# Kernel tuning notes

Measured on AMD Instinct MI355X. Metric: run time of the kernel, lower is better.

## Reference

```python
import jax, jax.numpy as jnp
import numpy as np

B, S, D, H, DK, FF, NQ = 4, 1024, 512, 64, 8, 2048, 8


def _layernorm(x, w, b, eps=1e-5):
    m = x.mean(-1, keepdims=True)
    v = ((x - m) ** 2).mean(-1, keepdims=True)
    return (x - m) / jnp.sqrt(v + eps) * w + b


def setup_inputs() -> dict:
    key = jax.random.key(0)
    ks = jax.random.split(key, 24)
    std = 0.02
    inp = {
        "x": jax.random.normal(ks[0], (B, S, D), dtype=jnp.float32),
        "Wq": jax.random.normal(ks[1], (D, D)) * std,
        "bq": jnp.zeros((D,)),
        "Wk": jax.random.normal(ks[2], (D, D)) * std,
        "bk": jnp.zeros((D,)),
        "Wv": jax.random.normal(ks[3], (D, D)) * std,
        "bv": jnp.zeros((D,)),
        "theta_attn": jax.random.normal(ks[4], (DK,)) * 0.1,  # trainable RX angles
        "gate_attn": jnp.asarray(1.0, dtype=jnp.float32),
        "Wo": jax.random.normal(ks[5], (D, D)) * std,
        "bo": jnp.zeros((D,)),
        "ln1_w": jnp.ones((D,)),
        "ln1_b": jnp.zeros((D,)),
        "W1": jax.random.normal(ks[6], (FF, NQ)) * std,
        "b1": jnp.zeros((FF,)),
        "W2": jax.random.normal(ks[7], (D, FF)) * std,
        "b2": jnp.zeros((D,)),
        "phi_ffn": jax.random.normal(ks[8], (NQ,)) * 0.1,  # trainable RY angles
        "gate_ffn": jnp.asarray(1.0, dtype=jnp.float32),
        "ln2_w": jnp.ones((D,)),
        "ln2_b": jnp.zeros((D,)),
    }
    return inp


def _attention(x, Wq, bq, Wk, bk, Wv, bv, theta, gate, Wo, bo):
    q = x @ Wq.T + bq
    k = x @ Wk.T + bk
    v = x @ Wv.T + bv
    sep = lambda t: t.reshape(B, S, H, DK).transpose(0, 2, 1, 3)  # [B,H,S,DK]
    qh, kh, vh = sep(q), sep(k), sep(v)
    scores = jnp.einsum("bhsd,bhtd->bhst", qh, kh) / np.sqrt(DK)
    probs = jax.nn.softmax(scores, axis=-1)
    classical = jnp.einsum("bhst,bhtd->bhsd", probs, vh)
    classical = classical.transpose(0, 2, 1, 3).reshape(B, S, D)
    # Quantum head: RX(x_i) then RX(theta_i) -> RX(x_i+theta_i), CNOT ring, <Z_j>.
    # Analytic expectations: <Z_0> = prod_{k=1..DK-1} cos(a_k);
    #                        <Z_j> = prod_{k=0..j}    cos(a_k)   (j >= 1).
    cos_a = jnp.cos(qh + theta)  # [B,H,S,DK]
    cp = jnp.cumprod(cos_a, axis=-1)
    z0 = jnp.prod(cos_a[..., 1:], axis=-1, keepdims=True)
    quantum = jnp.concatenate([z0, cp[..., 1:]], axis=-1)  # [B,H,S,DK]
    quantum = quantum.transpose(0, 2, 1, 3).reshape(B, S, D)
    out = gate * quantum + (1.0 - gate) * classical
    return out @ Wo.T + bo


def _ffn(x, W1, b1, W2, b2, phi, gate):
    xs = x[..., :NQ]  # encoder uses first NQ features
    # Quantum: RX(x_i) then RY(phi_i), measure <Z_i> = cos(x_i)*cos(phi_i).
    qm = jnp.cos(xs) * jnp.cos(phi)
    quantum = jax.nn.relu(qm @ W1.T + b1) @ W2.T + b2
    classical = jax.nn.relu(xs @ W1.T + b1) @ W2.T + b2
    return gate * quantum + (1.0 - gate) * classical


def reference(x, Wq, bq, Wk, bk, Wv, bv, theta_attn, gate_attn, Wo, bo,
              ln1_w, ln1_b, W1, b1, W2, b2, phi_ffn, gate_ffn, ln2_w, ln2_b):
    attn_out = _attention(x, Wq, bq, Wk, bk, Wv, bv, theta_attn, gate_attn, Wo, bo)
    x1 = _layernorm(x + attn_out, ln1_w, ln1_b)
    ffn_out = _ffn(x1, W1, b1, W2, b2, phi_ffn, gate_ffn)
    return _layernorm(x1 + ffn_out, ln2_w, ln2_b)
```

## Files before the change

### kernel.cpp

```cpp
#include <hip/hip_runtime.h>
#include <hip/hip_bf16.h>


typedef short short8 __attribute__((ext_vector_type(8)));
typedef float floatx4 __attribute__((ext_vector_type(4)));

__device__ __forceinline__ unsigned short f2bf_bits(float f) {
  __hip_bfloat16 h = __float2bfloat16(f);
  return *reinterpret_cast<unsigned short*>(&h);
}
__device__ __forceinline__ float bfbits2f(unsigned short u) {
  union { unsigned int u; float f; } c;
  c.u = (unsigned int)u << 16;
  return c.f;
}

#define GLOBAL_LOAD_LDS16(g, l)                                               \
  __builtin_amdgcn_global_load_lds(                                           \
      (const __attribute__((address_space(1))) void*)(g),                     \
      (__attribute__((address_space(3))) void*)(l), 16, 0, 0)

#define WAIT_VMCNT0()   asm volatile("s_waitcnt vmcnt(0)" ::: "memory")
#define WAIT_VMCNT8()   asm volatile("s_waitcnt vmcnt(8)" ::: "memory")
#define WAIT_VMCNT10()  asm volatile("s_waitcnt vmcnt(10)" ::: "memory")
#define WAIT_VMCNT16()  asm volatile("s_waitcnt vmcnt(16)" ::: "memory")
#define WAIT_VMCNT32()  asm volatile("s_waitcnt vmcnt(32)" ::: "memory")
#define WAIT_LGKM0()    asm volatile("s_waitcnt lgkmcnt(0)" ::: "memory")
#define BARRIER()       __builtin_amdgcn_s_barrier()

__device__ __forceinline__ void gemm_core(
    const __hip_bfloat16* __restrict__ A,
    const __hip_bfloat16* __restrict__ W,
    int K, long m0, long n0, int lane,
    __hip_bfloat16* sh, floatx4 acc[4][4])
{
  const int srow = lane >> 3;
  const int gchunk = (lane & 7) ^ srow;
  const int frow = lane & 15;
  const int fk = lane >> 4;

  auto stage = [&](int kt, __hip_bfloat16* buf) {
#pragma unroll
    for (int ib = 0; ib < 8; ++ib) {
      const int row = ib * 8 + srow;
      GLOBAL_LOAD_LDS16(A + (m0 + row) * K + kt + gchunk * 8, buf + ib * 512);
      GLOBAL_LOAD_LDS16(W + (n0 + row) * K + kt + gchunk * 8, buf + 4096 + ib * 512);
    }
  };

  const int ntiles = K >> 6;
  WAIT_LGKM0();
  stage(0, sh);
  if (ntiles > 1) stage(64, sh + 8192);
  if (ntiles > 2) stage(128, sh + 16384);

  for (int t = 0; t < ntiles; ++t) {
    __hip_bfloat16* buf = sh + (t % 3) * 8192;
    const int ahead = (ntiles - 1 - t) < 2 ? (ntiles - 1 - t) : 2;
    if (ahead == 2) { WAIT_VMCNT32(); }
    else if (ahead == 1) { WAIT_VMCNT16(); }
    else { WAIT_VMCNT0(); }

    short8 af[2][4], bf[2][4];
#pragma unroll
    for (int ks = 0; ks < 2; ++ks)
#pragma unroll
      for (int i = 0; i < 4; ++i) {
        const int ar = i * 16 + frow;
        af[ks][i] = *(const short8*)(buf + ar * 64 + (((ks * 4 + fk) ^ (ar & 7)) << 3));
        bf[ks][i] = *(const short8*)(buf + 4096 + ar * 64 + (((ks * 4 + fk) ^ (ar & 7)) << 3));
      }
    WAIT_LGKM0();
    if (t + 3 < ntiles) stage((t + 3) << 6, buf);
#pragma unroll
    for (int ks = 0; ks < 2; ++ks)
#pragma unroll
      for (int i = 0; i < 4; ++i)
#pragma unroll
        for (int j = 0; j < 4; ++j)
          acc[i][j] = __builtin_amdgcn_mfma_f32_16x16x32_bf16(
              af[ks][i], bf[ks][j], acc[i][j], 0, 0, 0);
  }
}

__device__ __forceinline__ void store_f32(
    floatx4 acc[4][4], float* __restrict__ C, const float* __restrict__ bias,
    long m0, long n0, int lane)
{
  const int col_l = lane & 15;
  const int row_l = (lane >> 4) << 2;
#pragma unroll
  for (int j = 0; j < 4; ++j) {
    const long col = n0 + j * 16 + col_l;
    const float bv = bias[col];
#pragma unroll
    for (int i = 0; i < 4; ++i)
#pragma unroll
      for (int r = 0; r < 4; ++r)
        C[(m0 + i * 16 + row_l + r) * 512 + col] = acc[i][j][r] + bv;
  }
}

__device__ __forceinline__ void store_bf16(
    floatx4 acc[4][4], __hip_bfloat16* __restrict__ C,
    const float* __restrict__ bias, long m0, long n0, int lane)
{
  const int col_l = lane & 15;
  const int row_l = (lane >> 4) << 2;
#pragma unroll
  for (int j = 0; j < 4; ++j) {
    const long col = n0 + j * 16 + col_l;
    const float bv = bias[col];
#pragma unroll
    for (int i = 0; i < 4; ++i)
#pragma unroll
      for (int r = 0; r < 4; ++r)
        C[(m0 + i * 16 + row_l + r) * 512 + col] =
            __float2bfloat16(acc[i][j][r] + bv);
  }
}

__global__ __launch_bounds__(64) void gemm_qkv(
    const __hip_bfloat16* __restrict__ x_bf,
    const __hip_bfloat16* __restrict__ Wq,
    const __hip_bfloat16* __restrict__ Wk,
    const __hip_bfloat16* __restrict__ Wv,
    const float* __restrict__ bq, const float* __restrict__ bk,
    const float* __restrict__ bvv,
    __hip_bfloat16* __restrict__ mix,
    float* __restrict__ Qb, float* __restrict__ Kb, float* __restrict__ Vb,
    const float* __restrict__ theta, const float* __restrict__ gateA)
{
  const int z = blockIdx.z;
  const float g = *gateA;
  if (z > 0 && g == 1.0f) return;
  const __hip_bfloat16* W = (z == 0) ? Wq : (z == 1) ? Wk : Wv;
  const float* bias = (z == 0) ? bq : (z == 1) ? bk : bvv;
  float* Cf = (z == 0) ? Qb : (z == 1) ? Kb : Vb;

  __shared__ __align__(16) __hip_bfloat16 sh[24576];
  const int lane = threadIdx.x;
  const long m0 = (long)blockIdx.x * 64;
  const long n0 = (long)blockIdx.y * 64;
  floatx4 acc[4][4];
#pragma unroll
  for (int i = 0; i < 4; ++i)
#pragma unroll
    for (int j = 0; j < 4; ++j) acc[i][j] = (floatx4){0.f, 0.f, 0.f, 0.f};

  gemm_core(x_bf, W, 512, m0, n0, lane, sh, acc);

  const int col_l = lane & 15;
  const int row_l = (lane >> 4) << 2;

  if (z > 0 || g != 1.0f) store_f32(acc, Cf, bias, m0, n0, lane);
  if (z == 0) {
    float* shf = (float*)sh;
    WAIT_LGKM0();
#pragma unroll
    for (int j = 0; j < 4; ++j) {
      const long col = n0 + j * 16 + col_l;
      const float bv = bias[col];
#pragma unroll
      for (int i = 0; i < 4; ++i)
#pragma unroll
        for (int r = 0; r < 4; ++r)
          shf[(i * 16 + row_l + r) * 64 + j * 16 + col_l] = acc[i][j][r] + bv;
    }
    WAIT_LGKM0();
    float th[8];
#pragma unroll
    for (int i = 0; i < 8; ++i) th[i] = theta[i];
#pragma unroll
    for (int t = 0; t < 8; ++t) {
      const int gidx = t * 64 + lane;
      const int row = gidx >> 3;
      const int hh = gidx & 7;
      const float* src = shf + row * 64 + hh * 8;
      float c[8];
#pragma unroll
      for (int i = 0; i < 8; ++i) c[i] = __cosf(src[i] + th[i]);
      float o[8];
      float p = c[1];
#pragma unroll
      for (int i = 2; i < 8; ++i) p *= c[i];
      o[0] = p;
      float cp = c[0];
#pragma unroll
      for (int i = 1; i < 8; ++i) { cp *= c[i]; o[i] = cp; }
      union { unsigned short u16[8]; uint4 v; } pk;
#pragma unroll
      for (int i = 0; i < 8; ++i) pk.u16[i] = f2bf_bits(o[i]);
      *(uint4*)(mix + (m0 + row) * 512 + n0 + hh * 8) = pk.v;
    }
  }
}

__global__ __launch_bounds__(512) void wo_lnffn(
    const __hip_bfloat16* __restrict__ A,
    const __hip_bfloat16* __restrict__ W,
    const float* __restrict__ bo,
    const float* __restrict__ x,
    const float* __restrict__ lw, const float* __restrict__ lb,
    float* __restrict__ x1, const float* __restrict__ phi,
    const float* __restrict__ W1,
    const float* __restrict__ b1,
    __hip_bfloat16* __restrict__ hq, __hip_bfloat16* __restrict__ hc,
    const float* __restrict__ gateF)
{
  __shared__ __align__(16) __hip_bfloat16 sh[68608];
  const int tid = threadIdx.x;
  const int wid = tid >> 6;
  const int lane = tid & 63;
  const long m0 = (long)blockIdx.x * 16;
  const long n0w = (long)wid * 64;

  const int srow = lane >> 3;
  const int gchunk = (lane & 7) ^ srow;
  const int frow = lane & 15;
  const int fk = lane >> 4;

  __hip_bfloat16* shA = sh;
  __hip_bfloat16* shW = sh + 3072 + wid * 8192;

  auto stageA = [&](int kt, int slot) {
    __hip_bfloat16* buf = shA + slot * 1024;
#pragma unroll
    for (int i = 0; i < 2; ++i) {
      const int row = i * 8 + srow;
      GLOBAL_LOAD_LDS16(A + (m0 + row) * 512 + kt + gchunk * 8, buf + i * 512);
    }
  };
  auto stageW = [&](int kt, int slot) {
    __hip_bfloat16* buf = shW + slot * 4096;
#pragma unroll
    for (int i = 0; i < 8; ++i) {
      const int row = i * 8 + srow;
      GLOBAL_LOAD_LDS16(W + (n0w + row) * 512 + kt + gchunk * 8, buf + i * 512);
    }
  };

  floatx4 acc[4];
#pragma unroll
  for (int j = 0; j < 4; ++j) acc[j] = (floatx4){0.f, 0.f, 0.f, 0.f};

  if (wid == 0) stageA(0, 0);
  stageW(0, 0);
  if (wid == 0) stageA(64, 1);
  stageW(64, 1);

  for (int t = 0; t < 8; ++t) {
    const int wslot = t & 1;
    const int aslot = t % 3;
    if (t < 7) { if (wid == 0) WAIT_VMCNT10(); else WAIT_VMCNT8(); }
    else       { WAIT_VMCNT0(); }
    BARRIER();

    short8 af[2], bf[2][4];
#pragma unroll
    for (int ks = 0; ks < 2; ++ks) {
      af[ks] = *(const short8*)(shA + aslot * 1024 + frow * 64 +
                                (((ks * 4 + fk) ^ (frow & 7)) << 3));
#pragma unroll
      for (int j = 0; j < 4; ++j) {
        const int wr = j * 16 + frow;
        bf[ks][j] = *(const short8*)(shW + wslot * 4096 + wr * 64 +
                                     (((ks * 4 + fk) ^ (frow & 7)) << 3));
      }
    }
    WAIT_LGKM0();
    if (t < 6) {
      if (wid == 0) stageA((t + 2) << 6, (t + 2) % 3);
      stageW((t + 2) << 6, wslot);
    }
#pragma unroll
    for (int ks = 0; ks < 2; ++ks)
#pragma unroll
      for (int j = 0; j < 4; ++j)
        acc[j] = __builtin_amdgcn_mfma_f32_16x16x32_bf16(
            af[ks], bf[ks][j], acc[j], 0, 0, 0);
  }

  BARRIER();

  float* attnL = (float*)sh;
  float* qmL = attnL + 16 * 516;
  float* xsL = qmL + 128;
  {
    const int col_l = lane & 15;
    const int row_l = (lane >> 4) << 2;
#pragma unroll
    for (int j = 0; j < 4; ++j) {
      const int c = (int)n0w + j * 16 + col_l;
      const float bv = bo[c];
#pragma unroll
      for (int r = 0; r < 4; ++r)
        attnL[(row_l + r) * 516 + c] = acc[j][r] + bv;
    }
  }
  WAIT_LGKM0();
  BARRIER();

  const int rr = tid >> 5;
  const int cl = tid & 31;
  const long rowg = m0 + rr;
  float sv[16];
  float sum = 0.f, ssq = 0.f;
#pragma unroll
  for (int i = 0; i < 16; ++i) {
    const int c = cl + i * 32;
    const float v = x[rowg * 512 + c] + attnL[rr * 516 + c];
    sv[i] = v; sum += v; ssq += v * v;
  }
#pragma unroll
  for (int off = 16; off > 0; off >>= 1) {
    sum += __shfl_xor(sum, off, 32);
    ssq += __shfl_xor(ssq, off, 32);
  }
  const float mean = sum * (1.0f / 512.0f);
  const float var = ssq * (1.0f / 512.0f) - mean * mean;
  const float rstd = rsqrtf(fmaxf(var, 0.0f) + 1e-5f);
#pragma unroll
  for (int i = 0; i < 16; ++i) {
    const int c = cl + i * 32;
    const float o = (sv[i] - mean) * rstd * lw[c] + lb[c];
    x1[rowg * 512 + c] = o;
    if (i == 0 && cl < 8) {
      qmL[rr * 8 + cl] = __cosf(o) * __cosf(phi[cl]);
      xsL[rr * 8 + cl] = o;
    }
  }
  WAIT_LGKM0();
  BARRIER();

  const int n4 = tid << 2;
  float w1r[4][8];
#pragma unroll
  for (int jr = 0; jr < 4; ++jr) {
    float4 wa = *(const float4*)(W1 + (long)(n4 + jr) * 8);
    float4 wb = *(const float4*)(W1 + (long)(n4 + jr) * 8 + 4);
    w1r[jr][0] = wa.x; w1r[jr][1] = wa.y; w1r[jr][2] = wa.z; w1r[jr][3] = wa.w;
    w1r[jr][4] = wb.x; w1r[jr][5] = wb.y; w1r[jr][6] = wb.z; w1r[jr][7] = wb.w;
  }
  float4 bb = *(const float4*)(b1 + n4);
  const float b1a[4] = {bb.x, bb.y, bb.z, bb.w};
  const float gv = *gateF;
#pragma unroll 2
  for (int r = 0; r < 16; ++r) {
    float qm8[8];
#pragma unroll
    for (int k = 0; k < 8; ++k) qm8[k] = qmL[r * 8 + k];
    union { unsigned short u16[4]; ushort4 v; } pk;
#pragma unroll
    for (int jr = 0; jr < 4; ++jr) {
      float a = b1a[jr];
#pragma unroll
      for (int k = 0; k < 8; ++k) a += qm8[k] * w1r[jr][k];
      pk.u16[jr] = f2bf_bits(fmaxf(a, 0.0f));
    }
    *(ushort4*)(hq + (m0 + r) * 2048 + n4) = pk.v;
    if (gv != 1.0f) {
      float xs8[8];
#pragma unroll
      for (int k = 0; k < 8; ++k) xs8[k] = xsL[r * 8 + k];
#pragma unroll
      for (int jr = 0; jr < 4; ++jr) {
        float a = b1a[jr];
#pragma unroll
        for (int k = 0; k < 8; ++k) a += xs8[k] * w1r[jr][k];
        pk.u16[jr] = f2bf_bits(fmaxf(a, 0.0f));
      }
      *(ushort4*)(hc + (m0 + r) * 2048 + n4) = pk.v;
    }
  }
}

__global__ __launch_bounds__(64) void gemm_ffnout(
    const __hip_bfloat16* __restrict__ hq,
    const __hip_bfloat16* __restrict__ hc,
    const __hip_bfloat16* __restrict__ W2, const float* __restrict__ b2,
    __hip_bfloat16* __restrict__ Fb, __hip_bfloat16* __restrict__ Fc,
    const float* __restrict__ gateF)
{
  const int z = blockIdx.z;
  if (z == 1 && *gateF == 1.0f) return;
  const __hip_bfloat16* A = z ? hc : hq;
  __hip_bfloat16* C = z ? Fc : Fb;
  __shared__ __align__(16) __hip_bfloat16 sh[24576];
  const int lane = threadIdx.x;
  const long m0 = (long)blockIdx.x * 64;
  const long n0 = (long)blockIdx.y * 64;
  floatx4 acc[4][4];
#pragma unroll
  for (int i = 0; i < 4; ++i)
#pragma unroll
    for (int j = 0; j < 4; ++j) acc[i][j] = (floatx4){0.f, 0.f, 0.f, 0.f};
  gemm_core(A, W2, 2048, m0, n0, lane, sh, acc);
  store_bf16(acc, C, b2, m0, n0, lane);
}

__device__ __forceinline__ void cvt_one(const float* s, __hip_bfloat16* d, int n,
                                        long tid, long stride) {
  const int n4 = n >> 2;
  for (long i = tid; i < n4; i += stride) {
    float4 v = ((const float4*)s)[i];
    ushort4 u;
    u.x = f2bf_bits(v.x); u.y = f2bf_bits(v.y);
    u.z = f2bf_bits(v.z); u.w = f2bf_bits(v.w);
    ((ushort4*)d)[i] = u;
  }
}

__global__ __launch_bounds__(256) void prep_inputs(
    const float* x, __hip_bfloat16* x_bf,
    const float* Wq, __hip_bfloat16* Wq_bf,
    const float* Wo, __hip_bfloat16* Wo_bf,
    const float* W2, __hip_bfloat16* W2_bf,
    const float* Wk, __hip_bfloat16* Wk_bf,
    const float* Wv, __hip_bfloat16* Wv_bf,
    const float* gateA)
{
  const long stride = (long)gridDim.x * blockDim.x;
  const long tid = (long)blockIdx.x * blockDim.x + threadIdx.x;
  cvt_one(x, x_bf, 4096 * 512, tid, stride);
  cvt_one(Wq, Wq_bf, 512 * 512, tid, stride);
  cvt_one(Wo, Wo_bf, 512 * 512, tid, stride);
  cvt_one(W2, W2_bf, 512 * 2048, tid, stride);
  if (*gateA != 1.0f) {
    cvt_one(Wk, Wk_bf, 512 * 512, tid, stride);
    cvt_one(Wv, Wv_bf, 512 * 512, tid, stride);
  }
}

__global__ __launch_bounds__(256) void attn_blend(
    const float* __restrict__ Qb, const float* __restrict__ Kb,
    const float* __restrict__ Vb, __hip_bfloat16* __restrict__ mix,
    const float* __restrict__ gateA)
{
  const float g = *gateA;
  if (g == 1.0f) return;
  const int idx = blockIdx.x * blockDim.x + threadIdx.x;
  if (idx >= 4 * 64 * 1024) return;
  const int s = idx & 1023;
  const int h = (idx >> 10) & 63;
  const int b = idx >> 16;
  const long qoff = ((long)(b * 1024 + s)) * 512 + h * 8;
  float q[8];
#pragma unroll
  for (int i = 0; i < 8; ++i) q[i] = Qb[qoff + i] * 0.35355339059327373f;
  float m = -INFINITY, l = 0.0f, acc[8];
#pragma unroll
  for (int i = 0; i < 8; ++i) acc[i] = 0.0f;
  for (int t = 0; t < 1024; ++t) {
    const long koff = ((long)(b * 1024 + t)) * 512 + h * 8;
    const float* kr = Kb + koff;
    const float* vr = Vb + koff;
    float sc = 0.0f;
#pragma unroll
    for (int i = 0; i < 8; ++i) sc += q[i] * kr[i];
    float nm = fmaxf(m, sc);
    float corr = __expf(m - nm);
    float p = __expf(sc - nm);
    l = l * corr + p;
#pragma unroll
    for (int i = 0; i < 8; ++i) acc[i] = acc[i] * corr + p * vr[i];
    m = nm;
  }
  const float inv = 1.0f / l;
  union { unsigned short u16[8]; uint4 v; } pk;
  pk.v = *(const uint4*)(mix + qoff);
#pragma unroll
  for (int i = 0; i < 8; ++i) {
    float quant = bfbits2f(pk.u16[i]);
    pk.u16[i] = f2bf_bits(g * quant + (1.0f - g) * acc[i] * inv);
  }
  *(uint4*)(mix + qoff) = pk.v;
}

__global__ __launch_bounds__(256) void add_ln3(
    const float* __restrict__ x1, const __hip_bfloat16* __restrict__ Fb,
    const __hip_bfloat16* __restrict__ Fc, const float* __restrict__ gateF,
    const float* __restrict__ lw, const float* __restrict__ lb,
    float* __restrict__ out)
{
  const int tid = threadIdx.x;
  const int wv = tid >> 6, lane = tid & 63;
  const int row = blockIdx.x * 4 + wv;
  const long base = (long)row * 512;
  const int c0 = lane * 8;
  float4 a0 = *(const float4*)(x1 + base + c0);
  float4 a1 = *(const float4*)(x1 + base + c0 + 4);
  union { unsigned short u16[8]; uint4 v; } fb;
  fb.v = *(const uint4*)(Fb + base + c0);
  const float xa[8] = {a0.x, a0.y, a0.z, a0.w, a1.x, a1.y, a1.z, a1.w};
  float s[8];
  const float gv = *gateF;
  if (gv != 1.0f) {
    union { unsigned short u16[8]; uint4 v; } fc;
    fc.v = *(const uint4*)(Fc + base + c0);
    const float om = 1.0f - gv;
#pragma unroll
    for (int i = 0; i < 8; ++i)
      s[i] = xa[i] + gv * bfbits2f(fb.u16[i]) + om * bfbits2f(fc.u16[i]);
  } else {
#pragma unroll
    for (int i = 0; i < 8; ++i) s[i] = xa[i] + bfbits2f(fb.u16[i]);
  }
  float sum = 0.f, ssq = 0.f;
#pragma unroll
  for (int i = 0; i < 8; ++i) { sum += s[i]; ssq += s[i] * s[i]; }
#pragma unroll
  for (int off = 32; off > 0; off >>= 1) {
    sum += __shfl_xor(sum, off);
    ssq += __shfl_xor(ssq, off);
  }
  const float mean = sum * (1.0f / 512.0f);
  const float var = ssq * (1.0f / 512.0f) - mean * mean;
  const float rstd = rsqrtf(fmaxf(var, 0.0f) + 1e-5f);
  float4 w0 = *(const float4*)(lw + c0);
  float4 w1 = *(const float4*)(lw + c0 + 4);
  float4 g0 = *(const float4*)(lb + c0);
  float4 g1 = *(const float4*)(lb + c0 + 4);
  const float wf[8] = {w0.x, w0.y, w0.z, w0.w, w1.x, w1.y, w1.z, w1.w};
  const float gf8[8] = {g0.x, g0.y, g0.z, g0.w, g1.x, g1.y, g1.z, g1.w};
  float o[8];
#pragma unroll
  for (int i = 0; i < 8; ++i) o[i] = (s[i] - mean) * rstd * wf[i] + gf8[i];
  *(float4*)(out + base + c0) = (float4){o[0], o[1], o[2], o[3]};
  *(float4*)(out + base + c0 + 4) = (float4){o[4], o[5], o[6], o[7]};
}

extern "C" void kernel_launch(void* const* d_in, const int* in_sizes, int n_in,
                              void* d_out, int out_size, void* d_ws, size_t ws_size,
                              hipStream_t stream) {
  const float* x     = (const float*)d_in[0];
  const float* Wq    = (const float*)d_in[1];
  const float* bq    = (const float*)d_in[2];
  const float* Wk    = (const float*)d_in[3];
  const float* bk    = (const float*)d_in[4];
  const float* Wv    = (const float*)d_in[5];
  const float* bv    = (const float*)d_in[6];
  const float* theta = (const float*)d_in[7];
  const float* gateA = (const float*)d_in[8];
  const float* Wo    = (const float*)d_in[9];
  const float* bo    = (const float*)d_in[10];
  const float* ln1w  = (const float*)d_in[11];
  const float* ln1b  = (const float*)d_in[12];
  const float* W1    = (const float*)d_in[13];
  const float* b1    = (const float*)d_in[14];
  const float* W2    = (const float*)d_in[15];
  const float* b2    = (const float*)d_in[16];
  const float* phi   = (const float*)d_in[17];
  const float* gateF = (const float*)d_in[18];
  const float* ln2w  = (const float*)d_in[19];
  const float* ln2b  = (const float*)d_in[20];
  float* out = (float*)d_out;

  const size_t MB = 1024 * 1024;
  char* wsb = (char*)d_ws;
  __hip_bfloat16* x_bf    = (__hip_bfloat16*)(wsb + 0 * MB);
  __hip_bfloat16* Wq_bf   = (__hip_bfloat16*)(wsb + 4 * MB);
  __hip_bfloat16* Wo_bf   = (__hip_bfloat16*)(wsb + 4 * MB + 512 * 1024);
  __hip_bfloat16* W2_bf   = (__hip_bfloat16*)(wsb + 5 * MB);
  __hip_bfloat16* mix_bf  = (__hip_bfloat16*)(wsb + 8 * MB);
  float*          x1      = (float*)(wsb + 16 * MB);
  __hip_bfloat16* hq_bf   = (__hip_bfloat16*)(wsb + 24 * MB);
  __hip_bfloat16* Fb_bf   = (__hip_bfloat16*)(wsb + 40 * MB);
  float*          Qb      = (float*)(wsb + 52 * MB);
  __hip_bfloat16* Wk_bf   = (__hip_bfloat16*)(wsb + 60 * MB);
  __hip_bfloat16* Wv_bf   = (__hip_bfloat16*)(wsb + 60 * MB + 512 * 1024);
  float*          Kb2     = (float*)(wsb + 61 * MB);
  float*          Vb2     = (float*)(wsb + 69 * MB);
  __hip_bfloat16* hc_bf   = (__hip_bfloat16*)(wsb + 77 * MB);
  __hip_bfloat16* Fc_bf   = (__hip_bfloat16*)(wsb + 93 * MB);

  prep_inputs<<<1024, 256, 0, stream>>>(
      x, x_bf, Wq, Wq_bf, Wo, Wo_bf, W2, W2_bf, Wk, Wk_bf, Wv, Wv_bf, gateA);
  gemm_qkv<<<dim3(64, 8, 3), 64, 0, stream>>>(
      x_bf, Wq_bf, Wk_bf, Wv_bf, bq, bk, bv,
      mix_bf, Qb, Kb2, Vb2, theta, gateA);
  attn_blend<<<1024, 256, 0, stream>>>(Qb, Kb2, Vb2, mix_bf, gateA);
  wo_lnffn<<<256, 512, 0, stream>>>(
      mix_bf, Wo_bf, bo, x, ln1w, ln1b, x1, phi, W1, b1, hq_bf, hc_bf, gateF);
  gemm_ffnout<<<dim3(64, 8, 2), 64, 0, stream>>>(
      hq_bf, hc_bf, W2_bf, b2, Fb_bf, Fc_bf, gateF);
  add_ln3<<<1024, 256, 0, stream>>>(x1, Fb_bf, Fc_bf, gateF, ln2w, ln2b, out);
}
```

Measured before the change: 152.7 us.

## Split K across two wavefronts in QKV and FFN-out GEMMs with LDS reduction

Each 64x64 GEMM tile block now runs two wavefronts, each handling half of the K dimension with its own double-buffered LDS staging area, replacing the single-wave triple-buffered loop. The partial accumulators from the second wave are written to LDS and added by the first wave after a barrier. The aim is more in-flight work per block and per CU for these latency-bound small-grid GEMMs, at the cost of a shallower prefetch depth, a larger LDS footprint per block, and an extra reduction step.

Result: faster. 146.3 us (-4.1%).

```diff
diff --git a/kernel.cpp b/kernel.cpp
--- a/kernel.cpp
+++ b/kernel.cpp
@@ -24,14 +24,14 @@
 #define WAIT_VMCNT8()   asm volatile("s_waitcnt vmcnt(8)" ::: "memory")
 #define WAIT_VMCNT10()  asm volatile("s_waitcnt vmcnt(10)" ::: "memory")
 #define WAIT_VMCNT16()  asm volatile("s_waitcnt vmcnt(16)" ::: "memory")
-#define WAIT_VMCNT32()  asm volatile("s_waitcnt vmcnt(32)" ::: "memory")
 #define WAIT_LGKM0()    asm volatile("s_waitcnt lgkmcnt(0)" ::: "memory")
 #define BARRIER()       __builtin_amdgcn_s_barrier()
-
-__device__ __forceinline__ void gemm_core(
+#define CFENCE()        asm volatile("" ::: "memory")
+
+__device__ __forceinline__ void gemm_core_ks(
     const __hip_bfloat16* __restrict__ A,
     const __hip_bfloat16* __restrict__ W,
-    int K, long m0, long n0, int lane,
+    int K, int kbeg, int ntiles, long m0, long n0, int lane,
     __hip_bfloat16* sh, floatx4 acc[4][4])
 {
   const int srow = lane >> 3;
@@ -48,18 +48,14 @@
     }
   };
 
-  const int ntiles = K >> 6;
   WAIT_LGKM0();
-  stage(0, sh);
-  if (ntiles > 1) stage(64, sh + 8192);
-  if (ntiles > 2) stage(128, sh + 16384);
+  stage(kbeg, sh);
+  if (ntiles > 1) stage(kbeg + 64, sh + 8192);
 
   for (int t = 0; t < ntiles; ++t) {
-    __hip_bfloat16* buf = sh + (t % 3) * 8192;
-    const int ahead = (ntiles - 1 - t) < 2 ? (ntiles - 1 - t) : 2;
-    if (ahead == 2) { WAIT_VMCNT32(); }
-    else if (ahead == 1) { WAIT_VMCNT16(); }
-    else { WAIT_VMCNT0(); }
+    __hip_bfloat16* buf = sh + (t & 1) * 8192;
+    if (t < ntiles - 1) { WAIT_VMCNT16(); }
+    else               { WAIT_VMCNT0(); }
 
     short8 af[2][4], bf[2][4];
 #pragma unroll
@@ -71,7 +67,7 @@
         bf[ks][i] = *(const short8*)(buf + 4096 + ar * 64 + (((ks * 4 + fk) ^ (ar & 7)) << 3));
       }
     WAIT_LGKM0();
-    if (t + 3 < ntiles) stage((t + 3) << 6, buf);
+    if (t + 2 < ntiles) stage(kbeg + ((t + 2) << 6), buf);
 #pragma unroll
     for (int ks = 0; ks < 2; ++ks)
 #pragma unroll
@@ -83,6 +79,28 @@
   }
 }
 
+__device__ __forceinline__ bool ks_reduce(
+    floatx4 acc[4][4], __hip_bfloat16* sh, int wid, int lane)
+{
+  float* red = (float*)(sh + 16384);
+  if (wid == 1) {
+#pragma unroll
+    for (int i = 0; i < 4; ++i)
+#pragma unroll
+      for (int j = 0; j < 4; ++j)
+        *(floatx4*)(red + ((i * 4 + j) * 64 + lane) * 4) = acc[i][j];
+    WAIT_LGKM0();
+  }
+  CFENCE(); BARRIER(); CFENCE();
+  if (wid == 1) return false;
+#pragma unroll
+  for (int i = 0; i < 4; ++i)
+#pragma unroll
+    for (int j = 0; j < 4; ++j)
+      acc[i][j] += *(const floatx4*)(red + ((i * 4 + j) * 64 + lane) * 4);
+  return true;
+}
+
 __device__ __forceinline__ void store_f32(
     floatx4 acc[4][4], float* __restrict__ C, const float* __restrict__ bias,
     long m0, long n0, int lane)
@@ -120,7 +138,7 @@
   }
 }
 
-__global__ __launch_bounds__(64) void gemm_qkv(
+__global__ __launch_bounds__(128) void gemm_qkv(
     const __hip_bfloat16* __restrict__ x_bf,
     const __hip_bfloat16* __restrict__ Wq,
     const __hip_bfloat16* __restrict__ Wk,
@@ -138,8 +156,10 @@
   const float* bias = (z == 0) ? bq : (z == 1) ? bk : bvv;
   float* Cf = (z == 0) ? Qb : (z == 1) ? Kb : Vb;
 
-  __shared__ __align__(16) __hip_bfloat16 sh[24576];
-  const int lane = threadIdx.x;
+  __shared__ __align__(16) __hip_bfloat16 sh[32768];
+  const int tid = threadIdx.x;
+  const int wid = tid >> 6;
+  const int lane = tid & 63;
   const long m0 = (long)blockIdx.x * 64;
   const long n0 = (long)blockIdx.y * 64;
   floatx4 acc[4][4];
@@ -148,7 +168,8 @@
 #pragma unroll
     for (int j = 0; j < 4; ++j) acc[i][j] = (floatx4){0.f, 0.f, 0.f, 0.f};
 
-  gemm_core(x_bf, W, 512, m0, n0, lane, sh, acc);
+  gemm_core_ks(x_bf, W, 512, wid * 256, 4, m0, n0, lane, sh + wid * 16384, acc);
+  if (!ks_reduce(acc, sh, wid, lane)) return;
 
   const int col_l = lane & 15;
   const int row_l = (lane >> 4) << 2;
@@ -375,7 +396,7 @@
   }
 }
 
-__global__ __launch_bounds__(64) void gemm_ffnout(
+__global__ __launch_bounds__(128) void gemm_ffnout(
     const __hip_bfloat16* __restrict__ hq,
     const __hip_bfloat16* __restrict__ hc,
     const __hip_bfloat16* __restrict__ W2, const float* __restrict__ b2,
@@ -386,8 +407,10 @@
   if (z == 1 && *gateF == 1.0f) return;
   const __hip_bfloat16* A = z ? hc : hq;
   __hip_bfloat16* C = z ? Fc : Fb;
-  __shared__ __align__(16) __hip_bfloat16 sh[24576];
-  const int lane = threadIdx.x;
+  __shared__ __align__(16) __hip_bfloat16 sh[32768];
+  const int tid = threadIdx.x;
+  const int wid = tid >> 6;
+  const int lane = tid & 63;
   const long m0 = (long)blockIdx.x * 64;
   const long n0 = (long)blockIdx.y * 64;
   floatx4 acc[4][4];
@@ -395,7 +418,8 @@
   for (int i = 0; i < 4; ++i)
 #pragma unroll
     for (int j = 0; j < 4; ++j) acc[i][j] = (floatx4){0.f, 0.f, 0.f, 0.f};
-  gemm_core(A, W2, 2048, m0, n0, lane, sh, acc);
+  gemm_core_ks(A, W2, 2048, wid * 1024, 16, m0, n0, lane, sh + wid * 16384, acc);
+  if (!ks_reduce(acc, sh, wid, lane)) return;
   store_bf16(acc, C, b2, m0, n0, lane);
 }
 
@@ -576,13 +600,13 @@
 
   prep_inputs<<<1024, 256, 0, stream>>>(
       x, x_bf, Wq, Wq_bf, Wo, Wo_bf, W2, W2_bf, Wk, Wk_bf, Wv, Wv_bf, gateA);
-  gemm_qkv<<<dim3(64, 8, 3), 64, 0, stream>>>(
+  gemm_qkv<<<dim3(64, 8, 3), 128, 0, stream>>>(
       x_bf, Wq_bf, Wk_bf, Wv_bf, bq, bk, bv,
       mix_bf, Qb, Kb2, Vb2, theta, gateA);
   attn_blend<<<1024, 256, 0, stream>>>(Qb, Kb2, Vb2, mix_bf, gateA);
   wo_lnffn<<<256, 512, 0, stream>>>(
       mix_bf, Wo_bf, bo, x, ln1w, ln1b, x1, phi, W1, b1, hq_bf, hc_bf, gateF);
-  gemm_ffnout<<<dim3(64, 8, 2), 64, 0, stream>>>(
+  gemm_ffnout<<<dim3(64, 8, 2), 128, 0, stream>>>(
       hq_bf, hc_bf, W2_bf, b2, Fb_bf, Fc_bf, gateF);
   add_ln3<<<1024, 256, 0, stream>>>(x1, Fb_bf, Fc_bf, gateF, ln2w, ln2b, out);
 }
```
